# Kernel optimization log

Measured on AMD Instinct MI355X. Metric: run time of the kernel, lower is better.

## Reference

```python
import jax, jax.numpy as jnp
import numpy as np

TEMPERATURE = 0.2
NUM_CLASSES = 80  # background label == NUM_CLASSES
M, K, B = 8192, 128, 60


def setup_inputs() -> dict:
    key = jax.random.key(0)
    k1, k2, k3 = jax.random.split(key, 3)
    feats = jax.random.normal(k1, (M, K), dtype=jnp.float32)
    feats = feats / jnp.linalg.norm(feats, axis=-1, keepdims=True)
    protos = jax.random.normal(k2, (B, K), dtype=jnp.float32)
    protos = protos / jnp.linalg.norm(protos, axis=-1, keepdims=True)
    labels = jax.random.randint(k3, (M,), 0, NUM_CLASSES + 1)  # NUM_CLASSES == bg
    proto_labels = jnp.arange(B, dtype=jnp.int64 if jax.config.read('jax_enable_x64') else jnp.int32)
    return {"features": feats, "labels": labels, "protos": protos, "proto_labels": proto_labels}


def reference(features, labels, protos, proto_labels):
    # masked (fixed-shape) formulation of the original boolean-gather code
    fg = labels != NUM_CLASSES                                   # [M]
    is_base = fg & jnp.any(labels[None, :] == proto_labels[:, None], axis=0)
    is_novel = fg & ~is_base
    nf = is_novel.astype(features.dtype)                         # [M] novel mask
    bf = is_base.astype(features.dtype)                          # [M] base mask
    numel = jnp.sum(fg).astype(features.dtype)

    sim = jnp.matmul(features, features.T) / TEMPERATURE          # [M,M]
    pk = jnp.matmul(features, protos.T) / TEMPERATURE             # [M,B]
    exp_sim = jnp.exp(sim)                                        # [M,M]
    eye = jnp.eye(features.shape[0], dtype=features.dtype)
    offdiag = (1.0 - eye)

    # ---- novel branch: rows i with is_novel[i] ----
    # denom: sum over novel j != i of exp(sim) + sum over protos of RAW pk (faithful to source)
    exp_nn_sum = jnp.sum(exp_sim * nf[None, :] * offdiag, axis=1)  # [M]
    denom_n = exp_nn_sum + jnp.sum(pk, axis=1)                     # [M]
    log_prob = sim - jnp.log(denom_n)[:, None]
    # novel_label_mask in source is elementwise labels==labels -> all True
    n_novel = jnp.sum(nf)
    cnt = jnp.maximum(n_novel - 1.0, 1.0)                          # per-row positive count
    per_row_novel = -jnp.sum(log_prob * nf[None, :] * offdiag, axis=1) / cnt
    loss_novel = jnp.sum(per_row_novel * nf)
    loss_novel = jnp.where(n_novel > 1.0, loss_novel, 0.0)

    # ---- base branch: rows i with is_base[i] ----
    safe_lab = jnp.clip(labels, 0, protos.shape[0] - 1)
    pi = jnp.einsum('nc,nc->n', features, protos[safe_lab]) / TEMPERATURE  # [M]
    denom_b = jnp.sum(exp_sim * nf[None, :], axis=1) + jnp.sum(jnp.exp(pk), axis=1)
    loss_base = jnp.sum(bf * -(pi - jnp.log(denom_b)))
    loss_base = jnp.where(jnp.any(is_base), loss_base, 0.0)

    return (loss_novel + loss_base) / numel
```

## Files before the change

kernel.cpp:

```cpp
#include <hip/hip_runtime.h>
#include <math.h>

#define NCLS 80
#define KDIM 128
#define INV_T 5.0f

typedef __attribute__((ext_vector_type(4))) float  floatx4;
typedef __attribute__((ext_vector_type(8))) short  short8;

__device__ inline unsigned short f2bf(float x) {
    unsigned int u = __float_as_uint(x);
    u += 0x7fffu + ((u >> 16) & 1u);
    return (unsigned short)(u >> 16);
}
__device__ inline short8 pack8(float4 a, float4 b) {
    short8 o;
    o[0] = (short)f2bf(a.x); o[1] = (short)f2bf(a.y);
    o[2] = (short)f2bf(a.z); o[3] = (short)f2bf(a.w);
    o[4] = (short)f2bf(b.x); o[5] = (short)f2bf(b.y);
    o[6] = (short)f2bf(b.z); o[7] = (short)f2bf(b.w);
    return o;
}
__device__ inline void g2lds16(const void* g, void* l) {
    __builtin_amdgcn_global_load_lds(
        (const __attribute__((address_space(1))) void*)g,
        (__attribute__((address_space(3))) void*)l, 16, 0, 0);
}

__global__ __launch_bounds__(256) void setup_kernel(
    const float* __restrict__ feats, const int* __restrict__ labels,
    const float* __restrict__ protos, int M, int B,
    int* __restrict__ novel_idx, int* __restrict__ counters,
    float* __restrict__ S1, float* __restrict__ T1,
    float* __restrict__ PKr, float* __restrict__ EK, float* __restrict__ out,
    unsigned short* __restrict__ Fb, unsigned short* __restrict__ Pb)
{
    const int i = blockIdx.x * 256 + threadIdx.x;
    const int T = gridDim.x * 256;
    if (i == 0) out[0] = 0.f;
    if (i < M) {
        S1[i] = 0.f; T1[i] = 0.f; PKr[i] = 0.f; EK[i] = 0.f;
        int lab = labels[i];
        bool fg  = (lab != NCLS);
        bool isb = fg && (lab >= 0) && (lab < B);
        bool isn = fg && !isb;
        if (isn) { int p = atomicAdd(&counters[0], 1); novel_idx[p] = i; }
        if (fg)  atomicAdd(&counters[1], 1);
        if (isb) atomicAdd(&counters[2], 1);
    }
    const int nch = (M + 1) * (KDIM / 8);
    for (int ch = i; ch < nch; ch += T) {
        short8 o = (short8)0;
        if (ch < M * (KDIM / 8)) {
            const float4* f4 = (const float4*)feats + (size_t)ch * 2;
            o = pack8(f4[0], f4[1]);
        }
        *(short8*)&Fb[(size_t)ch * 8] = o;
    }
    for (int ch = i; ch < 128 * (KDIM / 8); ch += T) {
        short8 o = (short8)0;
        if (ch < B * (KDIM / 8)) {
            const float4* f4 = (const float4*)protos + (size_t)ch * 2;
            o = pack8(f4[0], f4[1]);
        }
        *(short8*)&Pb[(size_t)ch * 8] = o;
    }
}

__global__ __launch_bounds__(256, 2) void gemm_kernel(
    const unsigned short* __restrict__ Fb, const unsigned short* __restrict__ Pb,
    const int* __restrict__ novel_idx, const int* __restrict__ counters,
    int M, int B,
    float* __restrict__ S1, float* __restrict__ T1,
    float* __restrict__ PKr, float* __restrict__ EK)
{
    __shared__ unsigned short As[128 * 128];
    __shared__ unsigned short Bs[128 * 128];
    __shared__ int nidx[128];

    const int Nn = counters[0];
    const int ntiles = (Nn + 127) >> 7;
    const int ct = blockIdx.x >> 6;
    const int rt = blockIdx.x & 63;
    if (ct > ntiles) return;
    const bool isproto = (ct == ntiles);
    const int row0 = rt * 128;
    const int tid = threadIdx.x;
    const int wbase = tid & ~63;

    {
        const unsigned short* a0 = Fb + (size_t)row0 * KDIM;
        #pragma unroll
        for (int p = 0; p < 8; ++p) {
            int Lc = p * 256 + tid;
            int r = Lc >> 4, c = Lc & 15;
            int cs = c ^ (r & 15);
            g2lds16(a0 + r * KDIM + cs * 8, As + (size_t)(p * 256 + wbase) * 8);
        }
    }
    {
        #pragma unroll
        for (int p = 0; p < 8; ++p) {
            int Lc = p * 256 + tid;
            int r = Lc >> 4, c = Lc & 15;
            int cs = c ^ (r & 15);
            const unsigned short* base;
            int nid;
            if (isproto) { base = Pb; nid = r; }
            else {
                base = Fb;
                int jg = ct * 128 + r;
                nid = (jg < Nn) ? novel_idx[jg] : M;
            }
            g2lds16(base + (size_t)nid * KDIM + cs * 8,
                    Bs + (size_t)(p * 256 + wbase) * 8);
        }
    }
    if (tid < 128) {
        int nid = -1;
        if (isproto) { if (tid < B) nid = tid; }
        else { int jg = ct * 128 + tid; if (jg < Nn) nid = novel_idx[jg]; }
        nidx[tid] = nid;
    }
    __syncthreads();

    const int wave = tid >> 6;
    const int lane = tid & 63;
    const int lr   = lane & 15;
    const int quad = lane >> 4;
    const int wrow = (wave >> 1) * 64;
    const int wcol = (wave & 1) * 64;

    floatx4 acc[4][4];
    #pragma unroll
    for (int r = 0; r < 4; ++r)
        #pragma unroll
        for (int c = 0; c < 4; ++c)
            acc[r][c] = (floatx4){0.f, 0.f, 0.f, 0.f};

    #pragma unroll
    for (int ks = 0; ks < 4; ++ks) {
        short8 a[4], b[4];
        #pragma unroll
        for (int r = 0; r < 4; ++r) {
            int row = wrow + r * 16 + lr;
            int phys = (ks * 4 + quad) ^ lr;
            a[r] = *(const short8*)&As[row * KDIM + phys * 8];
        }
        #pragma unroll
        for (int c = 0; c < 4; ++c) {
            int row = wcol + c * 16 + lr;
            int phys = (ks * 4 + quad) ^ lr;
            b[c] = *(const short8*)&Bs[row * KDIM + phys * 8];
        }
        #pragma unroll
        for (int r = 0; r < 4; ++r)
            #pragma unroll
            for (int c = 0; c < 4; ++c)
                acc[r][c] = __builtin_amdgcn_mfma_f32_16x16x32_bf16(
                    a[r], b[c], acc[r][c], 0, 0, 0);
    }

    int ncol[4];
    #pragma unroll
    for (int c = 0; c < 4; ++c) ncol[c] = nidx[wcol + c * 16 + lr];

    #pragma unroll
    for (int r = 0; r < 4; ++r) {
        int ibase = row0 + wrow + r * 16 + quad * 4;
        #pragma unroll
        for (int reg = 0; reg < 4; ++reg) {
            int irow = ibase + reg;
            float se = 0.f, sr = 0.f;
            #pragma unroll
            for (int c = 0; c < 4; ++c) {
                float sim = acc[r][c][reg] * INV_T;
                bool valid = (ncol[c] >= 0) && (isproto || ncol[c] != irow);
                if (valid) { se += __expf(sim); sr += sim; }
            }
            #pragma unroll
            for (int off = 1; off < 16; off <<= 1) {
                se += __shfl_xor(se, off);
                sr += __shfl_xor(sr, off);
            }
            if (lr == 0) {
                if (isproto) { atomicAdd(&EK[irow], se); atomicAdd(&PKr[irow], sr); }
                else         { atomicAdd(&S1[irow], se); atomicAdd(&T1[irow], sr); }
            }
        }
    }
}

__global__ __launch_bounds__(256) void finalize_kernel(
    const float* __restrict__ feats, const float* __restrict__ protos,
    const int* __restrict__ labels,
    const float* __restrict__ S1, const float* __restrict__ T1,
    const float* __restrict__ PKr, const float* __restrict__ EK,
    const int* __restrict__ counters, int M, int B, float* __restrict__ out)
{
    __shared__ float part[16];
    const int tid  = threadIdx.x;
    const int rloc = tid >> 4;
    const int q    = tid & 15;
    const int row  = blockIdx.x * 16 + rloc;
    const int rs   = min(row, M - 1);

    const int Nn = counters[0], numel = counters[1], nbase = counters[2];

    int lab = labels[rs];
    bool fg  = (lab != NCLS);
    bool isb = fg && (lab >= 0) && (lab < B);
    bool isn = fg && !isb;
    int  sl  = min(max(lab, 0), B - 1);

    float d = 0.f;
    #pragma unroll
    for (int j = 0; j < 8; ++j) {
        int k = q + j * 16;
        d += feats[(size_t)rs * KDIM + k] * protos[(size_t)sl * KDIM + k];
    }
    #pragma unroll
    for (int off = 1; off < 16; off <<= 1) d += __shfl_xor(d, off);

    if (q == 0) {
        float loss = 0.f;
        if (row < M) {
            if (isn && Nn > 1) {
                float cnt = (float)(Nn - 1);
                float dn  = S1[rs] + PKr[rs];
                loss = -(T1[rs] - cnt * logf(dn)) / cnt;
            } else if (isb && nbase > 0) {
                float pi = d * INV_T;
                float db = S1[rs] + EK[rs];
                loss = -(pi - logf(db));
            }
        }
        part[rloc] = loss;
    }
    __syncthreads();
    if (tid == 0) {
        float s = 0.f;
        #pragma unroll
        for (int r = 0; r < 16; ++r) s += part[r];
        atomicAdd(out, s / (float)numel);
    }
}

extern "C" void kernel_launch(void* const* d_in, const int* in_sizes, int n_in,
                              void* d_out, int out_size, void* d_ws, size_t ws_size,
                              hipStream_t stream)
{
    const float* feats  = (const float*)d_in[0];
    const int*   labels = (const int*)d_in[1];
    const float* protos = (const float*)d_in[2];

    const int M = in_sizes[1];
    const int B = in_sizes[3];

    char* ws = (char*)d_ws;
    int*   counters  = (int*)ws;
    float* S1  = (float*)(ws + 64);
    float* T1  = S1 + M;
    float* PKr = T1 + M;
    float* EK  = PKr + M;
    int*   novel_idx = (int*)(EK + M);
    unsigned short* Fb = (unsigned short*)(novel_idx + M);
    unsigned short* Pb = Fb + (size_t)(M + 1) * KDIM;

    hipMemsetAsync(counters, 0, 64, stream);

    setup_kernel<<<256, 256, 0, stream>>>(
        feats, labels, protos, M, B, novel_idx, counters,
        S1, T1, PKr, EK, (float*)d_out, Fb, Pb);

    int rowTiles = (M + 127) / 128;
    int maxct    = (M + 127) / 128;
    gemm_kernel<<<rowTiles * (maxct + 1), 256, 0, stream>>>(
        Fb, Pb, novel_idx, counters, M, B, S1, T1, PKr, EK);

    finalize_kernel<<<(M + 15) / 16, 256, 0, stream>>>(
        feats, protos, labels, S1, T1, PKr, EK, counters, M, B, (float*)d_out);
}
```

Baseline: 104.1 us.

## Use linearity for raw-sim sums and make GEMM blocks persistent with row-tile reuse

The raw similarity row sums (T1 and PKr) are no longer accumulated inside the GEMM. They are computed in finalize as dot products of each feature with the sum of novel features and the sum of prototypes, and those sums are reduced during setup. The GEMM now runs as a fixed grid of 512 blocks. Each block walks a contiguous range of tiles, reloads the A tile only when the row tile changes, and accumulates exp sums in registers so it flushes fewer atomics. This cuts epilogue work and launch waste from early-exit blocks, at the cost of a serialized tile loop with no load/compute overlap and slightly different float rounding in the linear sums.

```diff
diff --git a/kernel.cpp b/kernel.cpp
--- a/kernel.cpp
+++ b/kernel.cpp
@@ -31,15 +31,18 @@
     const float* __restrict__ feats, const int* __restrict__ labels,
     const float* __restrict__ protos, int M, int B,
     int* __restrict__ novel_idx, int* __restrict__ counters,
-    float* __restrict__ S1, float* __restrict__ T1,
-    float* __restrict__ PKr, float* __restrict__ EK, float* __restrict__ out,
+    float* __restrict__ S1, float* __restrict__ EK,
+    float* __restrict__ Fsum, float* __restrict__ Psum,
+    float* __restrict__ out,
     unsigned short* __restrict__ Fb, unsigned short* __restrict__ Pb)
 {
-    const int i = blockIdx.x * 256 + threadIdx.x;
+    __shared__ float sred[256][8];
+    const int tid = threadIdx.x;
+    const int i = blockIdx.x * 256 + tid;
     const int T = gridDim.x * 256;
     if (i == 0) out[0] = 0.f;
     if (i < M) {
-        S1[i] = 0.f; T1[i] = 0.f; PKr[i] = 0.f; EK[i] = 0.f;
+        S1[i] = 0.f; EK[i] = 0.f;
         int lab = labels[i];
         bool fg  = (lab != NCLS);
         bool isb = fg && (lab >= 0) && (lab < B);
@@ -48,22 +51,71 @@
         if (fg)  atomicAdd(&counters[1], 1);
         if (isb) atomicAdd(&counters[2], 1);
     }
+
+    float4 fa0 = make_float4(0.f, 0.f, 0.f, 0.f);
+    float4 fa1 = make_float4(0.f, 0.f, 0.f, 0.f);
     const int nch = (M + 1) * (KDIM / 8);
     for (int ch = i; ch < nch; ch += T) {
         short8 o = (short8)0;
         if (ch < M * (KDIM / 8)) {
             const float4* f4 = (const float4*)feats + (size_t)ch * 2;
-            o = pack8(f4[0], f4[1]);
+            float4 v0 = f4[0], v1 = f4[1];
+            o = pack8(v0, v1);
+            int lab = labels[ch >> 4];
+            bool isn = (lab != NCLS) && !((lab >= 0) && (lab < B));
+            if (isn) {
+                fa0.x += v0.x; fa0.y += v0.y; fa0.z += v0.z; fa0.w += v0.w;
+                fa1.x += v1.x; fa1.y += v1.y; fa1.z += v1.z; fa1.w += v1.w;
+            }
         }
         *(short8*)&Fb[(size_t)ch * 8] = o;
     }
-    for (int ch = i; ch < 128 * (KDIM / 8); ch += T) {
+    sred[tid][0] = fa0.x; sred[tid][1] = fa0.y; sred[tid][2] = fa0.z; sred[tid][3] = fa0.w;
+    sred[tid][4] = fa1.x; sred[tid][5] = fa1.y; sred[tid][6] = fa1.z; sred[tid][7] = fa1.w;
+    __syncthreads();
+    for (int s = 128; s >= 16; s >>= 1) {
+        if (tid < s) {
+            #pragma unroll
+            for (int j = 0; j < 8; ++j) sred[tid][j] += sred[tid + s][j];
+        }
+        __syncthreads();
+    }
+    if (tid < 16) {
+        #pragma unroll
+        for (int j = 0; j < 8; ++j) atomicAdd(&Fsum[tid * 8 + j], sred[tid][j]);
+    }
+
+    if (i < 128 * (KDIM / 8)) {
+        int r = i >> 4, c = i & 15;
         short8 o = (short8)0;
-        if (ch < B * (KDIM / 8)) {
-            const float4* f4 = (const float4*)protos + (size_t)ch * 2;
-            o = pack8(f4[0], f4[1]);
-        }
-        *(short8*)&Pb[(size_t)ch * 8] = o;
+        if (r < B) {
+            const float4* p4 = (const float4*)protos + (size_t)i * 2;
+            float4 v0 = p4[0], v1 = p4[1];
+            o = pack8(v0, v1);
+            atomicAdd(&Psum[c * 8 + 0], v0.x); atomicAdd(&Psum[c * 8 + 1], v0.y);
+            atomicAdd(&Psum[c * 8 + 2], v0.z); atomicAdd(&Psum[c * 8 + 3], v0.w);
+            atomicAdd(&Psum[c * 8 + 4], v1.x); atomicAdd(&Psum[c * 8 + 5], v1.y);
+            atomicAdd(&Psum[c * 8 + 6], v1.z); atomicAdd(&Psum[c * 8 + 7], v1.w);
+        }
+        *(short8*)&Pb[(size_t)i * 8] = o;
+    }
+}
+
+__device__ inline void flush_se(float se16[4][4], float* dest, int row0,
+                                int wrow, int quad, int lr, int M)
+{
+    #pragma unroll
+    for (int r = 0; r < 4; ++r) {
+        #pragma unroll
+        for (int reg = 0; reg < 4; ++reg) {
+            float v = se16[r][reg];
+            #pragma unroll
+            for (int off = 1; off < 16; off <<= 1) v += __shfl_xor(v, off);
+            if (lr == 0) {
+                int irow = row0 + wrow + r * 16 + quad * 4 + reg;
+                if (irow < M) atomicAdd(&dest[irow], v);
+            }
+        }
     }
 }
 
@@ -71,8 +123,7 @@
     const unsigned short* __restrict__ Fb, const unsigned short* __restrict__ Pb,
     const int* __restrict__ novel_idx, const int* __restrict__ counters,
     int M, int B,
-    float* __restrict__ S1, float* __restrict__ T1,
-    float* __restrict__ PKr, float* __restrict__ EK)
+    float* __restrict__ S1, float* __restrict__ EK)
 {
     __shared__ unsigned short As[128 * 128];
     __shared__ unsigned short Bs[128 * 128];
@@ -80,33 +131,63 @@
 
     const int Nn = counters[0];
     const int ntiles = (Nn + 127) >> 7;
-    const int ct = blockIdx.x >> 6;
-    const int rt = blockIdx.x & 63;
-    if (ct > ntiles) return;
-    const bool isproto = (ct == ntiles);
-    const int row0 = rt * 128;
+    const int width = ntiles + 1;
+    const int rtc = (M + 127) >> 7;
+    const long total = (long)rtc * width;
+    const int G = gridDim.x, b = blockIdx.x;
+    const int t0 = (int)(total * b / G);
+    const int t1 = (int)(total * (b + 1) / G);
+    if (t0 >= t1) return;
+
     const int tid = threadIdx.x;
     const int wbase = tid & ~63;
-
-    {
-        const unsigned short* a0 = Fb + (size_t)row0 * KDIM;
+    const int wave = tid >> 6, lane = tid & 63;
+    const int lr = lane & 15, quad = lane >> 4;
+    const int wrow = (wave >> 1) * 64, wcol = (wave & 1) * 64;
+
+    float se16[4][4];
+    float* pend = nullptr;
+    int pend_row0 = 0;
+    int cur_rt = -1;
+    bool first = true;
+
+    for (int t = t0; t < t1; ++t) {
+        const int rt = t / width, ct = t - rt * width;
+        const bool isp = (ct == ntiles);
+        const int row0 = rt * 128;
+        float* dest = isp ? EK : S1;
+
+        if (dest != pend || row0 != pend_row0) {
+            if (pend) flush_se(se16, pend, pend_row0, wrow, quad, lr, M);
+            #pragma unroll
+            for (int r = 0; r < 4; ++r)
+                #pragma unroll
+                for (int g = 0; g < 4; ++g) se16[r][g] = 0.f;
+            pend = dest; pend_row0 = row0;
+        }
+
+        if (!first) __syncthreads();
+        first = false;
+
+        if (rt != cur_rt) {
+            cur_rt = rt;
+            const unsigned short* a0 = Fb + (size_t)row0 * KDIM;
+            #pragma unroll
+            for (int p = 0; p < 8; ++p) {
+                int Lc = p * 256 + tid;
+                int r = Lc >> 4, c = Lc & 15;
+                int cs = c ^ (r & 15);
+                g2lds16(a0 + (size_t)r * KDIM + cs * 8,
+                        As + (size_t)(p * 256 + wbase) * 8);
+            }
+        }
         #pragma unroll
         for (int p = 0; p < 8; ++p) {
             int Lc = p * 256 + tid;
             int r = Lc >> 4, c = Lc & 15;
             int cs = c ^ (r & 15);
-            g2lds16(a0 + r * KDIM + cs * 8, As + (size_t)(p * 256 + wbase) * 8);
-        }
-    }
-    {
-        #pragma unroll
-        for (int p = 0; p < 8; ++p) {
-            int Lc = p * 256 + tid;
-            int r = Lc >> 4, c = Lc & 15;
-            int cs = c ^ (r & 15);
-            const unsigned short* base;
-            int nid;
-            if (isproto) { base = Pb; nid = r; }
+            const unsigned short* base; int nid;
+            if (isp) { base = Pb; nid = r; }
             else {
                 base = Fb;
                 int jg = ct * 128 + r;
@@ -115,87 +196,72 @@
             g2lds16(base + (size_t)nid * KDIM + cs * 8,
                     Bs + (size_t)(p * 256 + wbase) * 8);
         }
-    }
-    if (tid < 128) {
-        int nid = -1;
-        if (isproto) { if (tid < B) nid = tid; }
-        else { int jg = ct * 128 + tid; if (jg < Nn) nid = novel_idx[jg]; }
-        nidx[tid] = nid;
-    }
-    __syncthreads();
-
-    const int wave = tid >> 6;
-    const int lane = tid & 63;
-    const int lr   = lane & 15;
-    const int quad = lane >> 4;
-    const int wrow = (wave >> 1) * 64;
-    const int wcol = (wave & 1) * 64;
-
-    floatx4 acc[4][4];
-    #pragma unroll
-    for (int r = 0; r < 4; ++r)
-        #pragma unroll
-        for (int c = 0; c < 4; ++c)
-            acc[r][c] = (floatx4){0.f, 0.f, 0.f, 0.f};
-
-    #pragma unroll
-    for (int ks = 0; ks < 4; ++ks) {
-        short8 a[4], b[4];
+        if (tid < 128) {
+            int nid = -1;
+            if (isp) { if (tid < B) nid = tid; }
+            else { int jg = ct * 128 + tid; if (jg < Nn) nid = novel_idx[jg]; }
+            nidx[tid] = nid;
+        }
+        __syncthreads();
+
+        floatx4 acc[4][4];
+        #pragma unroll
+        for (int r = 0; r < 4; ++r)
+            #pragma unroll
+            for (int c = 0; c < 4; ++c)
+                acc[r][c] = (floatx4){0.f, 0.f, 0.f, 0.f};
+
+        #pragma unroll
+        for (int ks = 0; ks < 4; ++ks) {
+            short8 a[4], bfr[4];
+            #pragma unroll
+            for (int r = 0; r < 4; ++r) {
+                int row = wrow + r * 16 + lr;
+                int phys = (ks * 4 + quad) ^ lr;
+                a[r] = *(const short8*)&As[row * KDIM + phys * 8];
+            }
+            #pragma unroll
+            for (int c = 0; c < 4; ++c) {
+                int row = wcol + c * 16 + lr;
+                int phys = (ks * 4 + quad) ^ lr;
+                bfr[c] = *(const short8*)&Bs[row * KDIM + phys * 8];
+            }
+            #pragma unroll
+            for (int r = 0; r < 4; ++r)
+                #pragma unroll
+                for (int c = 0; c < 4; ++c)
+                    acc[r][c] = __builtin_amdgcn_mfma_f32_16x16x32_bf16(
+                        a[r], bfr[c], acc[r][c], 0, 0, 0);
+        }
+
+        int ncol[4];
+        #pragma unroll
+        for (int c = 0; c < 4; ++c) ncol[c] = nidx[wcol + c * 16 + lr];
         #pragma unroll
         for (int r = 0; r < 4; ++r) {
-            int row = wrow + r * 16 + lr;
-            int phys = (ks * 4 + quad) ^ lr;
-            a[r] = *(const short8*)&As[row * KDIM + phys * 8];
-        }
-        #pragma unroll
-        for (int c = 0; c < 4; ++c) {
-            int row = wcol + c * 16 + lr;
-            int phys = (ks * 4 + quad) ^ lr;
-            b[c] = *(const short8*)&Bs[row * KDIM + phys * 8];
-        }
-        #pragma unroll
-        for (int r = 0; r < 4; ++r)
-            #pragma unroll
-            for (int c = 0; c < 4; ++c)
-                acc[r][c] = __builtin_amdgcn_mfma_f32_16x16x32_bf16(
-                    a[r], b[c], acc[r][c], 0, 0, 0);
-    }
-
-    int ncol[4];
-    #pragma unroll
-    for (int c = 0; c < 4; ++c) ncol[c] = nidx[wcol + c * 16 + lr];
-
-    #pragma unroll
-    for (int r = 0; r < 4; ++r) {
-        int ibase = row0 + wrow + r * 16 + quad * 4;
-        #pragma unroll
-        for (int reg = 0; reg < 4; ++reg) {
-            int irow = ibase + reg;
-            float se = 0.f, sr = 0.f;
-            #pragma unroll
-            for (int c = 0; c < 4; ++c) {
-                float sim = acc[r][c][reg] * INV_T;
-                bool valid = (ncol[c] >= 0) && (isproto || ncol[c] != irow);
-                if (valid) { se += __expf(sim); sr += sim; }
-            }
-            #pragma unroll
-            for (int off = 1; off < 16; off <<= 1) {
-                se += __shfl_xor(se, off);
-                sr += __shfl_xor(sr, off);
-            }
-            if (lr == 0) {
-                if (isproto) { atomicAdd(&EK[irow], se); atomicAdd(&PKr[irow], sr); }
-                else         { atomicAdd(&S1[irow], se); atomicAdd(&T1[irow], sr); }
-            }
-        }
-    }
+            int ibase = row0 + wrow + r * 16 + quad * 4;
+            #pragma unroll
+            for (int reg = 0; reg < 4; ++reg) {
+                int irow = ibase + reg;
+                float se = 0.f;
+                #pragma unroll
+                for (int c = 0; c < 4; ++c) {
+                    float sim = acc[r][c][reg] * INV_T;
+                    bool valid = (ncol[c] >= 0) && (isp || ncol[c] != irow);
+                    if (valid) se += __expf(sim);
+                }
+                se16[r][reg] += se;
+            }
+        }
+    }
+    flush_se(se16, pend, pend_row0, wrow, quad, lr, M);
 }
 
 __global__ __launch_bounds__(256) void finalize_kernel(
     const float* __restrict__ feats, const float* __restrict__ protos,
     const int* __restrict__ labels,
-    const float* __restrict__ S1, const float* __restrict__ T1,
-    const float* __restrict__ PKr, const float* __restrict__ EK,
+    const float* __restrict__ S1, const float* __restrict__ EK,
+    const float* __restrict__ Fsum, const float* __restrict__ Psum,
     const int* __restrict__ counters, int M, int B, float* __restrict__ out)
 {
     __shared__ float part[16];
@@ -213,24 +279,35 @@
     bool isn = fg && !isb;
     int  sl  = min(max(lab, 0), B - 1);
 
-    float d = 0.f;
+    float dp = 0.f, dfs = 0.f, dps = 0.f, dsf = 0.f;
     #pragma unroll
     for (int j = 0; j < 8; ++j) {
         int k = q + j * 16;
-        d += feats[(size_t)rs * KDIM + k] * protos[(size_t)sl * KDIM + k];
+        float f = feats[(size_t)rs * KDIM + k];
+        dp  += f * protos[(size_t)sl * KDIM + k];
+        dfs += f * Fsum[k];
+        dps += f * Psum[k];
+        dsf += f * f;
     }
     #pragma unroll
-    for (int off = 1; off < 16; off <<= 1) d += __shfl_xor(d, off);
+    for (int off = 1; off < 16; off <<= 1) {
+        dp  += __shfl_xor(dp, off);
+        dfs += __shfl_xor(dfs, off);
+        dps += __shfl_xor(dps, off);
+        dsf += __shfl_xor(dsf, off);
+    }
 
     if (q == 0) {
         float loss = 0.f;
         if (row < M) {
             if (isn && Nn > 1) {
                 float cnt = (float)(Nn - 1);
-                float dn  = S1[rs] + PKr[rs];
-                loss = -(T1[rs] - cnt * logf(dn)) / cnt;
+                float T1  = (dfs - dsf) * INV_T;
+                float PKr = dps * INV_T;
+                float dn  = S1[rs] + PKr;
+                loss = -(T1 - cnt * logf(dn)) / cnt;
             } else if (isb && nbase > 0) {
-                float pi = d * INV_T;
+                float pi = dp * INV_T;
                 float db = S1[rs] + EK[rs];
                 loss = -(pi - logf(db));
             }
@@ -258,26 +335,24 @@
     const int B = in_sizes[3];
 
     char* ws = (char*)d_ws;
-    int*   counters  = (int*)ws;
-    float* S1  = (float*)(ws + 64);
-    float* T1  = S1 + M;
-    float* PKr = T1 + M;
-    float* EK  = PKr + M;
+    int*   counters = (int*)ws;
+    float* Fsum = (float*)(ws + 256);
+    float* Psum = (float*)(ws + 768);
+    float* S1  = (float*)(ws + 2048);
+    float* EK  = S1 + M;
     int*   novel_idx = (int*)(EK + M);
     unsigned short* Fb = (unsigned short*)(novel_idx + M);
     unsigned short* Pb = Fb + (size_t)(M + 1) * KDIM;
 
-    hipMemsetAsync(counters, 0, 64, stream);
+    hipMemsetAsync(ws, 0, 2048, stream);
 
     setup_kernel<<<256, 256, 0, stream>>>(
         feats, labels, protos, M, B, novel_idx, counters,
-        S1, T1, PKr, EK, (float*)d_out, Fb, Pb);
-
-    int rowTiles = (M + 127) / 128;
-    int maxct    = (M + 127) / 128;
-    gemm_kernel<<<rowTiles * (maxct + 1), 256, 0, stream>>>(
-        Fb, Pb, novel_idx, counters, M, B, S1, T1, PKr, EK);
+        S1, EK, Fsum, Psum, (float*)d_out, Fb, Pb);
+
+    gemm_kernel<<<512, 256, 0, stream>>>(
+        Fb, Pb, novel_idx, counters, M, B, S1, EK);
 
     finalize_kernel<<<(M + 15) / 16, 256, 0, stream>>>(
-        feats, protos, labels, S1, T1, PKr, EK, counters, M, B, (float*)d_out);
-}
+        feats, protos, labels, S1, EK, Fsum, Psum, counters, M, B, (float*)d_out);
+}
```

Result: slower. 145.5 us (+39.8%).

## Make GEMM kernel persistent with balanced tile ranges and per-run row accumulation

Applied to the files above, without the earlier changes.

Replaces the one-block-per-tile grid, where many blocks exit early because the novel count is known only at runtime, with a fixed 512-block persistent grid. Each block walks a contiguous range of (row tile, column tile) pairs. The A tile is reloaded only when the row tile changes, and row sums are kept in registers and flushed with atomics only when the run ends, which cuts atomic traffic. The tail of the work may be less evenly spread, and each tile now needs an extra barrier with no double buffering.

```diff
diff --git a/kernel.cpp b/kernel.cpp
--- a/kernel.cpp
+++ b/kernel.cpp
@@ -57,13 +57,36 @@
         }
         *(short8*)&Fb[(size_t)ch * 8] = o;
     }
-    for (int ch = i; ch < 128 * (KDIM / 8); ch += T) {
+    if (i < 128 * (KDIM / 8)) {
+        int r = i >> 4;
         short8 o = (short8)0;
-        if (ch < B * (KDIM / 8)) {
-            const float4* f4 = (const float4*)protos + (size_t)ch * 2;
-            o = pack8(f4[0], f4[1]);
-        }
-        *(short8*)&Pb[(size_t)ch * 8] = o;
+        if (r < B) {
+            const float4* p4 = (const float4*)protos + (size_t)i * 2;
+            o = pack8(p4[0], p4[1]);
+        }
+        *(short8*)&Pb[(size_t)i * 8] = o;
+    }
+}
+
+__device__ inline void flush_run(float se16[4][4], float sr16[4][4],
+                                 float* dE, float* dR, int row0,
+                                 int wrow, int quad, int lr, int M)
+{
+    #pragma unroll
+    for (int r = 0; r < 4; ++r) {
+        #pragma unroll
+        for (int reg = 0; reg < 4; ++reg) {
+            float ve = se16[r][reg], vr = sr16[r][reg];
+            #pragma unroll
+            for (int off = 1; off < 16; off <<= 1) {
+                ve += __shfl_xor(ve, off);
+                vr += __shfl_xor(vr, off);
+            }
+            if (lr == 0) {
+                int irow = row0 + wrow + r * 16 + quad * 4 + reg;
+                if (irow < M) { atomicAdd(&dE[irow], ve); atomicAdd(&dR[irow], vr); }
+            }
+        }
     }
 }
 
@@ -80,33 +103,64 @@
 
     const int Nn = counters[0];
     const int ntiles = (Nn + 127) >> 7;
-    const int ct = blockIdx.x >> 6;
-    const int rt = blockIdx.x & 63;
-    if (ct > ntiles) return;
-    const bool isproto = (ct == ntiles);
-    const int row0 = rt * 128;
+    const int width = ntiles + 1;
+    const int rtc = (M + 127) >> 7;
+    const long total = (long)rtc * width;
+    const int G = gridDim.x, b = blockIdx.x;
+    const int t0 = (int)(total * b / G);
+    const int t1 = (int)(total * (b + 1) / G);
+    if (t0 >= t1) return;
+
     const int tid = threadIdx.x;
     const int wbase = tid & ~63;
-
-    {
-        const unsigned short* a0 = Fb + (size_t)row0 * KDIM;
+    const int wave = tid >> 6, lane = tid & 63;
+    const int lr = lane & 15, quad = lane >> 4;
+    const int wrow = (wave >> 1) * 64, wcol = (wave & 1) * 64;
+
+    float se16[4][4], sr16[4][4];
+    int pend_row0 = -1;
+    bool pend_isp = false;
+    int cur_rt = -1;
+    bool first = true;
+
+    for (int t = t0; t < t1; ++t) {
+        const int rt = t / width, ct = t - rt * width;
+        const bool isp = (ct == ntiles);
+        const int row0 = rt * 128;
+
+        if (isp != pend_isp || row0 != pend_row0) {
+            if (pend_row0 >= 0)
+                flush_run(se16, sr16, pend_isp ? EK : S1, pend_isp ? PKr : T1,
+                          pend_row0, wrow, quad, lr, M);
+            #pragma unroll
+            for (int r = 0; r < 4; ++r)
+                #pragma unroll
+                for (int g = 0; g < 4; ++g) { se16[r][g] = 0.f; sr16[r][g] = 0.f; }
+            pend_isp = isp; pend_row0 = row0;
+        }
+
+        if (!first) __syncthreads();
+        first = false;
+
+        if (rt != cur_rt) {
+            cur_rt = rt;
+            const unsigned short* a0 = Fb + (size_t)row0 * KDIM;
+            #pragma unroll
+            for (int p = 0; p < 8; ++p) {
+                int Lc = p * 256 + tid;
+                int r = Lc >> 4, c = Lc & 15;
+                int cs = c ^ (r & 15);
+                g2lds16(a0 + (size_t)r * KDIM + cs * 8,
+                        As + (size_t)(p * 256 + wbase) * 8);
+            }
+        }
         #pragma unroll
         for (int p = 0; p < 8; ++p) {
             int Lc = p * 256 + tid;
             int r = Lc >> 4, c = Lc & 15;
             int cs = c ^ (r & 15);
-            g2lds16(a0 + r * KDIM + cs * 8, As + (size_t)(p * 256 + wbase) * 8);
-        }
-    }
-    {
-        #pragma unroll
-        for (int p = 0; p < 8; ++p) {
-            int Lc = p * 256 + tid;
-            int r = Lc >> 4, c = Lc & 15;
-            int cs = c ^ (r & 15);
-            const unsigned short* base;
-            int nid;
-            if (isproto) { base = Pb; nid = r; }
+            const unsigned short* base; int nid;
+            if (isp) { base = Pb; nid = r; }
             else {
                 base = Fb;
                 int jg = ct * 128 + r;
@@ -115,80 +169,68 @@
             g2lds16(base + (size_t)nid * KDIM + cs * 8,
                     Bs + (size_t)(p * 256 + wbase) * 8);
         }
-    }
-    if (tid < 128) {
-        int nid = -1;
-        if (isproto) { if (tid < B) nid = tid; }
-        else { int jg = ct * 128 + tid; if (jg < Nn) nid = novel_idx[jg]; }
-        nidx[tid] = nid;
-    }
-    __syncthreads();
-
-    const int wave = tid >> 6;
-    const int lane = tid & 63;
-    const int lr   = lane & 15;
-    const int quad = lane >> 4;
-    const int wrow = (wave >> 1) * 64;
-    const int wcol = (wave & 1) * 64;
-
-    floatx4 acc[4][4];
-    #pragma unroll
-    for (int r = 0; r < 4; ++r)
-        #pragma unroll
-        for (int c = 0; c < 4; ++c)
-            acc[r][c] = (floatx4){0.f, 0.f, 0.f, 0.f};
-
-    #pragma unroll
-    for (int ks = 0; ks < 4; ++ks) {
-        short8 a[4], b[4];
+        if (tid < 128) {
+            int nid = -1;
+            if (isp) { if (tid < B) nid = tid; }
+            else { int jg = ct * 128 + tid; if (jg < Nn) nid = novel_idx[jg]; }
+            nidx[tid] = nid;
+        }
+        __syncthreads();
+
+        floatx4 acc[4][4];
+        #pragma unroll
+        for (int r = 0; r < 4; ++r)
+            #pragma unroll
+            for (int c = 0; c < 4; ++c)
+                acc[r][c] = (floatx4){0.f, 0.f, 0.f, 0.f};
+
+        #pragma unroll
+        for (int ks = 0; ks < 4; ++ks) {
+            short8 a[4], bfr[4];
+            #pragma unroll
+            for (int r = 0; r < 4; ++r) {
+                int row = wrow + r * 16 + lr;
+                int phys = (ks * 4 + quad) ^ lr;
+                a[r] = *(const short8*)&As[row * KDIM + phys * 8];
+            }
+            #pragma unroll
+            for (int c = 0; c < 4; ++c) {
+                int row = wcol + c * 16 + lr;
+                int phys = (ks * 4 + quad) ^ lr;
+                bfr[c] = *(const short8*)&Bs[row * KDIM + phys * 8];
+            }
+            #pragma unroll
+            for (int r = 0; r < 4; ++r)
+                #pragma unroll
+                for (int c = 0; c < 4; ++c)
+                    acc[r][c] = __builtin_amdgcn_mfma_f32_16x16x32_bf16(
+                        a[r], bfr[c], acc[r][c], 0, 0, 0);
+        }
+
+        int ncol[4];
+        #pragma unroll
+        for (int c = 0; c < 4; ++c) ncol[c] = nidx[wcol + c * 16 + lr];
         #pragma unroll
         for (int r = 0; r < 4; ++r) {
-            int row = wrow + r * 16 + lr;
-            int phys = (ks * 4 + quad) ^ lr;
-            a[r] = *(const short8*)&As[row * KDIM + phys * 8];
-        }
-        #pragma unroll
-        for (int c = 0; c < 4; ++c) {
-            int row = wcol + c * 16 + lr;
-            int phys = (ks * 4 + quad) ^ lr;
-            b[c] = *(const short8*)&Bs[row * KDIM + phys * 8];
-        }
-        #pragma unroll
-        for (int r = 0; r < 4; ++r)
-            #pragma unroll
-            for (int c = 0; c < 4; ++c)
-                acc[r][c] = __builtin_amdgcn_mfma_f32_16x16x32_bf16(
-                    a[r], b[c], acc[r][c], 0, 0, 0);
-    }
-
-    int ncol[4];
-    #pragma unroll
-    for (int c = 0; c < 4; ++c) ncol[c] = nidx[wcol + c * 16 + lr];
-
-    #pragma unroll
-    for (int r = 0; r < 4; ++r) {
-        int ibase = row0 + wrow + r * 16 + quad * 4;
-        #pragma unroll
-        for (int reg = 0; reg < 4; ++reg) {
-            int irow = ibase + reg;
-            float se = 0.f, sr = 0.f;
-            #pragma unroll
-            for (int c = 0; c < 4; ++c) {
-                float sim = acc[r][c][reg] * INV_T;
-                bool valid = (ncol[c] >= 0) && (isproto || ncol[c] != irow);
-                if (valid) { se += __expf(sim); sr += sim; }
-            }
-            #pragma unroll
-            for (int off = 1; off < 16; off <<= 1) {
-                se += __shfl_xor(se, off);
-                sr += __shfl_xor(sr, off);
-            }
-            if (lr == 0) {
-                if (isproto) { atomicAdd(&EK[irow], se); atomicAdd(&PKr[irow], sr); }
-                else         { atomicAdd(&S1[irow], se); atomicAdd(&T1[irow], sr); }
-            }
-        }
-    }
+            int ibase = row0 + wrow + r * 16 + quad * 4;
+            #pragma unroll
+            for (int reg = 0; reg < 4; ++reg) {
+                int irow = ibase + reg;
+                float se = 0.f, sr = 0.f;
+                #pragma unroll
+                for (int c = 0; c < 4; ++c) {
+                    float sim = acc[r][c][reg] * INV_T;
+                    bool valid = (ncol[c] >= 0) && (isp || ncol[c] != irow);
+                    if (valid) { se += __expf(sim); sr += sim; }
+                }
+                se16[r][reg] += se;
+                sr16[r][reg] += sr;
+            }
+        }
+    }
+    if (pend_row0 >= 0)
+        flush_run(se16, sr16, pend_isp ? EK : S1, pend_isp ? PKr : T1,
+                  pend_row0, wrow, quad, lr, M);
 }
 
 __global__ __launch_bounds__(256) void finalize_kernel(
@@ -258,7 +300,7 @@
     const int B = in_sizes[3];
 
     char* ws = (char*)d_ws;
-    int*   counters  = (int*)ws;
+    int*   counters = (int*)ws;
     float* S1  = (float*)(ws + 64);
     float* T1  = S1 + M;
     float* PKr = T1 + M;
@@ -273,9 +315,7 @@
         feats, labels, protos, M, B, novel_idx, counters,
         S1, T1, PKr, EK, (float*)d_out, Fb, Pb);
 
-    int rowTiles = (M + 127) / 128;
-    int maxct    = (M + 127) / 128;
-    gemm_kernel<<<rowTiles * (maxct + 1), 256, 0, stream>>>(
+    gemm_kernel<<<512, 256, 0, stream>>>(
         Fb, Pb, novel_idx, counters, M, B, S1, T1, PKr, EK);
 
     finalize_kernel<<<(M + 15) / 16, 256, 0, stream>>>(
```

Result: faster. 99.12 us (-4.8%).
